# Performance work log

Hardware: AMD Instinct MI355X
Metric: run time of the kernel (lower is better)

Reference implementation:

```python
import jax, jax.numpy as jnp
import numpy as np

# ---- static config (from xib add_argument defaults / chosen production sizes) ----
B, L = 16, 50            # batch, text length
LU, KU, DIM = 60, 100, 60
V, MAXVL = 2000, 10      # vocab size, max vocab word length (J)
MIN_WL, MAX_WL = 4, 10   # min/max extracted word length
NE = MAX_WL - MIN_WL + 1 # number of len_e candidates
INS_DEL_COST = 3.5       # min_ins_del_cost
UNEXTRACTED_PROB = 0.01
CONTEXT_WEIGHT = 0.1     # weight for context (conv) log-probs
NEG = -9999.9


def setup_inputs() -> dict:
    key = jax.random.key(0)
    ks = jax.random.split(key, 8)
    unit_id_seqs = jax.random.randint(ks[0], (B, L), 0, LU)
    lengths = 10 + jax.random.randint(ks[1], (B,), 0, L - 9)  # in [10, L]
    unit_repr = jax.random.normal(ks[2], (KU, DIM), jnp.float32)
    aligner_weight = 0.1 * jax.random.normal(ks[3], (LU, KU), jnp.float32)
    conv_w = jax.random.normal(ks[4], (DIM, DIM, 3), jnp.float32) / np.sqrt(3.0 * DIM)
    conv_b = jnp.zeros((DIM,), jnp.float32)
    vocab_ids = jax.random.randint(ks[5], (V, MAXVL), 0, KU)
    vocab_lengths = MIN_WL + jax.random.randint(ks[6], (V,), 0, MAXVL - MIN_WL + 1)
    return dict(unit_id_seqs=unit_id_seqs, lengths=lengths, unit_repr=unit_repr,
                aligner_weight=aligner_weight, conv_w=conv_w, conv_b=conv_b,
                vocab_ids=vocab_ids, vocab_lengths=vocab_lengths)


def reference(unit_id_seqs, lengths, unit_repr, aligner_weight, conv_w, conv_b,
              vocab_ids, vocab_lengths):
    # ---- G2P layer: embedding-as-matmul + Conv1d over length ----
    ku_char_repr = aligner_weight @ unit_repr                 # (LU, DIM)
    emb = ku_char_repr[unit_id_seqs]                          # (B, L, DIM)
    x = jnp.swapaxes(emb, 1, 2)                               # (B, DIM, L)
    y = jax.lax.conv_general_dilated(x, conv_w, (1,), 'SAME',
                                     dimension_numbers=('NCH', 'OIH', 'NCH'))
    word_repr = jnp.swapaxes(y + conv_b[None, :, None], 1, 2)  # (B, L, DIM)
    char_log_probs = jax.nn.log_softmax(ku_char_repr @ unit_repr.T, axis=-1)  # (LU, KU)
    alignment = jnp.exp(char_log_probs)
    ctx_log_probs = jax.nn.log_softmax(word_repr @ unit_repr.T, axis=-1)      # (B, L, KU)
    # per-position substitution log prob against each known unit
    pos_lp = char_log_probs[unit_id_seqs] + CONTEXT_WEIGHT * ctx_log_probs    # (B, L, KU)
    sub = pos_lp[:, :, vocab_ids]                                             # (B, L, V, J)
    sub = jnp.pad(sub, ((0, 0), (0, MAX_WL), (0, 0), (0, 0)), constant_values=NEG)
    J = MAXVL
    # ---- edit-distance style DP over (span char i, vocab char j), vectorized
    # over (batch, start position, vocab). prev[b,s,j,v] = f[i-1][j].
    j_ar = jnp.arange(J + 1, dtype=sub.dtype)
    prev = jnp.broadcast_to((-INS_DEL_COST * j_ar)[None, None, :, None], (B, L, J + 1, V))
    vl_idx = jnp.broadcast_to(vocab_lengths[None, None, None, :].astype(jnp.int32), (B, L, 1, V))
    lls = []
    for i in range(1, MAX_WL + 1):          # fixed small loop (<=10)
        sub_i = sub[:, i - 1:i - 1 + L]     # (B, L, V, J): char at position s+i-1
        row = [jnp.full((B, L, V), -INS_DEL_COST * i, dtype=sub.dtype)]
        for j in range(1, J + 1):           # fixed small loop (<=10)
            diag = prev[:, :, j - 1, :] + sub_i[:, :, :, j - 1]
            up = prev[:, :, j, :] - INS_DEL_COST
            left = row[j - 1] - INS_DEL_COST
            row.append(jnp.maximum(diag, jnp.maximum(up, left)))
        prev = jnp.stack(row, axis=2)       # (B, L, J+1, V)
        if i >= MIN_WL:                     # matched ll for word length i
            lls.append(jnp.take_along_axis(prev, vl_idx, axis=2)[:, :, 0, :])
    ll = jnp.stack(lls, axis=2)             # (B, L, NE, V) = matches.ll
    # ---- viability mask + unextracted penalty, pick best candidate ----
    starts = jnp.arange(L)
    word_lens = MIN_WL + jnp.arange(NE)
    viable = (starts[None, :, None] + word_lens[None, None, :]) <= lengths[:, None, None]  # (B,L,NE)
    unextracted = (lengths[:, None, None] - word_lens[None, None, :]).astype(ll.dtype)     # (B,1,NE)
    score = (ll + jnp.where(viable, 0.0, NEG)[..., None]
             + (unextracted * np.log(UNEXTRACTED_PROB))[..., None, :, None][:, 0])
    flat = score.reshape(B, L * NE * V)
    best_idx = jnp.argmax(flat, axis=1)
    best_matched_ll = jnp.max(flat, axis=1)
    start = best_idx // (NE * V)
    e_idx = (best_idx // V) % NE
    best_matched_vocab = best_idx % V
    end = start + MIN_WL + e_idx - 1
    return start, end, best_matched_ll, best_matched_vocab, alignment
```

## Files before the change

### kernel.cpp

```cpp
#include <hip/hip_runtime.h>
#include <math.h>
#include <stdint.h>

#define B_ 16
#define L_ 50
#define LU_ 60
#define KU_ 100
#define DIM_ 60
#define V_ 2000
#define MAXVL_ 10
#define MIN_WL_ 4
#define MAX_WL_ 10
#define NE_ 7
#define IDC_ 3.5f
#define LOG_UNEXT_ (-4.6051701859880913680359829093687f)
#define CTXW_ 0.1f
#define NQ_ 13

#define WS_PLP  0
#define WS_BEST_BYTES (80000u * 4u)
#define BEST_STRIDE 8
#define WS_VPACK_BYTES (WS_BEST_BYTES + 1024u)

#define URP_ 61
#define CWP_ 61
#define TSP_ 12

__global__ __launch_bounds__(256) void ctx_kernel(
    const int* __restrict__ uid,
    const float* __restrict__ unit_repr,
    const float* __restrict__ aligner_w,
    const float* __restrict__ conv_w,
    const float* __restrict__ conv_b,
    const int* __restrict__ vocab_ids,
    const int* __restrict__ vocab_lengths,
    float* __restrict__ ws_plp,
    float* __restrict__ out_align,
    unsigned long long* __restrict__ g_best,
    int* __restrict__ vpack)
{
  int blk = blockIdx.x;
  int t = threadIdx.x;

  if (blk == B_ * NQ_) {
    __shared__ unsigned cnt[NE_];
    if (t < NE_) cnt[t] = 0u;
    __syncthreads();
    for (int v = t; v < V_; v += 256)
      atomicAdd(&cnt[vocab_lengths[v] - MIN_WL_], 1u);
    __syncthreads();
    if (t == 0) {
      unsigned s = 0;
      for (int e = 0; e < NE_; ++e) { unsigned c = cnt[e]; cnt[e] = s; s += c; }
    }
    __syncthreads();
    for (int v = t; v < V_; v += 256) {
      int vl = vocab_lengths[v];
      unsigned dst = atomicAdd(&cnt[vl - MIN_WL_], 1u);
      unsigned q0 = 0u, q1 = 0u, q2 = 0u;
#pragma unroll
      for (int j = 0; j < 4; ++j) q0 |= ((unsigned)vocab_ids[v * MAXVL_ + j]) << (j * 8);
#pragma unroll
      for (int j = 0; j < 4; ++j) q1 |= ((unsigned)vocab_ids[v * MAXVL_ + 4 + j]) << (j * 8);
#pragma unroll
      for (int j = 0; j < 2; ++j) q2 |= ((unsigned)vocab_ids[v * MAXVL_ + 8 + j]) << (j * 8);
      int4 w;
      w.x = (int)q0; w.y = (int)q1; w.z = (int)q2;
      w.w = (int)((unsigned)vl | ((unsigned)v << 8));
      ((int4*)vpack)[dst] = w;
    }
    return;
  }

  int b = blk / NQ_, q = blk % NQ_;
  int l0 = 4 * q;
  int npos = (l0 + 4 <= L_) ? 4 : (L_ - l0);
  int alr = (blk < LU_) ? blk : -1;

  __shared__ float s_ur[KU_ * URP_];
  __shared__ float s_cw[3 * DIM_ * CWP_];
  __shared__ float s_aw[7 * KU_];
  __shared__ float s_kx[7 * DIM_];
  __shared__ float swr[4 * DIM_];
  __shared__ float sclp[4 * KU_];
  __shared__ float sctx[4 * KU_];
  __shared__ float salg[KU_];
  __shared__ float sls[9];

  if (blk == 0 && t < B_) g_best[t * BEST_STRIDE] = 0ull;

  const float4* ur4 = (const float4*)unit_repr;
  for (int k = t; k < (KU_ * DIM_) / 4; k += 256) {
    float4 v = ur4[k];
    int i0 = 4 * k;
    s_ur[((i0 + 0) / DIM_) * URP_ + ((i0 + 0) % DIM_)] = v.x;
    s_ur[((i0 + 1) / DIM_) * URP_ + ((i0 + 1) % DIM_)] = v.y;
    s_ur[((i0 + 2) / DIM_) * URP_ + ((i0 + 2) % DIM_)] = v.z;
    s_ur[((i0 + 3) / DIM_) * URP_ + ((i0 + 3) % DIM_)] = v.w;
  }
  const float4* cw4 = (const float4*)conv_w;
  for (int k = t; k < (DIM_ * DIM_ * 3) / 4; k += 256) {
    float4 v = cw4[k];
    int i0 = 4 * k;
    float vv[4] = {v.x, v.y, v.z, v.w};
#pragma unroll
    for (int e = 0; e < 4; ++e) {
      int idx = i0 + e;
      int o = idx / (3 * DIM_), id = idx % (3 * DIM_);
      s_cw[id * CWP_ + o] = vv[e];
    }
  }
  for (int i = t; i < 7 * KU_; i += 256) {
    int m = i / KU_, k = i - m * KU_;
    float w = 0.f;
    if (m < 6) {
      int ld = l0 - 1 + m;
      if (ld >= 0 && ld < L_) {
        int u = uid[b * L_ + ld];
        w = aligner_w[u * KU_ + k];
      }
    } else if (alr >= 0) {
      w = aligner_w[alr * KU_ + k];
    }
    s_aw[i] = w;
  }
  __syncthreads();

  for (int idx = t; idx < 7 * DIM_; idx += 256) {
    int m = idx / DIM_, c = idx - m * DIM_;
    const float4* aw4 = (const float4*)&s_aw[m * KU_];
    float acc = 0.f;
    for (int k4 = 0; k4 < KU_ / 4; ++k4) {
      float4 a = aw4[k4];
      int k = 4 * k4;
      acc += a.x * s_ur[(k + 0) * URP_ + c];
      acc += a.y * s_ur[(k + 1) * URP_ + c];
      acc += a.z * s_ur[(k + 2) * URP_ + c];
      acc += a.w * s_ur[(k + 3) * URP_ + c];
    }
    s_kx[idx] = acc;
  }
  __syncthreads();

  for (int idx = t; idx < 240 + 4 * KU_; idx += 256) {
    if (idx < 240) {
      int p = idx / DIM_, o = idx - p * DIM_;
      const float4* x04 = (const float4*)&s_kx[(p + 0) * DIM_];
      const float4* x14 = (const float4*)&s_kx[(p + 1) * DIM_];
      const float4* x24 = (const float4*)&s_kx[(p + 2) * DIM_];
      float acc = conv_b[o];
      for (int i4 = 0; i4 < DIM_ / 4; ++i4) {
        float4 x0 = x04[i4], x1 = x14[i4], x2 = x24[i4];
        int i = 4 * i4;
        acc += x0.x * s_cw[((i + 0) * 3 + 0) * CWP_ + o];
        acc += x1.x * s_cw[((i + 0) * 3 + 1) * CWP_ + o];
        acc += x2.x * s_cw[((i + 0) * 3 + 2) * CWP_ + o];
        acc += x0.y * s_cw[((i + 1) * 3 + 0) * CWP_ + o];
        acc += x1.y * s_cw[((i + 1) * 3 + 1) * CWP_ + o];
        acc += x2.y * s_cw[((i + 1) * 3 + 2) * CWP_ + o];
        acc += x0.z * s_cw[((i + 2) * 3 + 0) * CWP_ + o];
        acc += x1.z * s_cw[((i + 2) * 3 + 1) * CWP_ + o];
        acc += x2.z * s_cw[((i + 2) * 3 + 2) * CWP_ + o];
        acc += x0.w * s_cw[((i + 3) * 3 + 0) * CWP_ + o];
        acc += x1.w * s_cw[((i + 3) * 3 + 1) * CWP_ + o];
        acc += x2.w * s_cw[((i + 3) * 3 + 2) * CWP_ + o];
      }
      swr[p * DIM_ + o] = acc;
    } else {
      int r = idx - 240;
      int p = r / KU_, j = r - p * KU_;
      const float4* kx4 = (const float4*)&s_kx[(p + 1) * DIM_];
      float acc = 0.f;
      for (int d4 = 0; d4 < DIM_ / 4; ++d4) {
        float4 x = kx4[d4];
        int d = 4 * d4;
        acc += x.x * s_ur[j * URP_ + d + 0];
        acc += x.y * s_ur[j * URP_ + d + 1];
        acc += x.z * s_ur[j * URP_ + d + 2];
        acc += x.w * s_ur[j * URP_ + d + 3];
      }
      sclp[r] = acc;
    }
  }
  __syncthreads();

  for (int idx = t; idx < 4 * KU_ + KU_; idx += 256) {
    if (idx < 4 * KU_) {
      int p = idx / KU_, j = idx - p * KU_;
      const float4* w4 = (const float4*)&swr[p * DIM_];
      float acc = 0.f;
      for (int d4 = 0; d4 < DIM_ / 4; ++d4) {
        float4 x = w4[d4];
        int d = 4 * d4;
        acc += x.x * s_ur[j * URP_ + d + 0];
        acc += x.y * s_ur[j * URP_ + d + 1];
        acc += x.z * s_ur[j * URP_ + d + 2];
        acc += x.w * s_ur[j * URP_ + d + 3];
      }
      sctx[idx] = acc;
    } else {
      int j = idx - 4 * KU_;
      const float4* kx4 = (const float4*)&s_kx[6 * DIM_];
      float acc = 0.f;
      for (int d4 = 0; d4 < DIM_ / 4; ++d4) {
        float4 x = kx4[d4];
        int d = 4 * d4;
        acc += x.x * s_ur[j * URP_ + d + 0];
        acc += x.y * s_ur[j * URP_ + d + 1];
        acc += x.z * s_ur[j * URP_ + d + 2];
        acc += x.w * s_ur[j * URP_ + d + 3];
      }
      salg[j] = acc;
    }
  }
  __syncthreads();

  {
    int g = t >> 5, lane = t & 31;
#pragma unroll
    for (int round = 0; round < 2; ++round) {
      int r = round * 8 + g;
      if (r < 9) {
        const float* arr = (r == 8) ? salg
                          : ((r & 1) ? &sctx[(r >> 1) * KU_] : &sclp[(r >> 1) * KU_]);
        float v1 = arr[lane];
        float v2 = arr[32 + lane];
        float v3 = arr[64 + lane];
        float v4 = (lane < KU_ - 96) ? arr[96 + lane] : -1e30f;
        float mx = fmaxf(fmaxf(v1, v2), fmaxf(v3, v4));
#pragma unroll
        for (int off = 16; off > 0; off >>= 1)
          mx = fmaxf(mx, __shfl_xor(mx, off));
        float s = expf(v1 - mx) + expf(v2 - mx) + expf(v3 - mx) +
                  ((lane < KU_ - 96) ? expf(v4 - mx) : 0.f);
#pragma unroll
        for (int off = 16; off > 0; off >>= 1)
          s += __shfl_xor(s, off);
        if (lane == 0) sls[r] = mx + logf(s);
      }
    }
  }
  __syncthreads();

  for (int idx = t; idx < 4 * KU_; idx += 256) {
    int p = idx / KU_, j = idx - p * KU_;
    if (p < npos) {
      float pos = (sclp[idx] - sls[2 * p]) + CTXW_ * (sctx[idx] - sls[2 * p + 1]);
      ws_plp[(b * L_ + l0 + p) * KU_ + j] = pos;
    }
  }
  if (alr >= 0 && t < KU_)
    out_align[alr * KU_ + t] = expf(salg[t] - sls[8]);
}

__global__ __launch_bounds__(256) void dp_kernel(
    const int* __restrict__ lengths,
    const float* __restrict__ ws_plp,
    const int* __restrict__ vpack,
    unsigned long long* __restrict__ g_best)
{
  int bl = blockIdx.x;
  int b = bl / L_, l = bl % L_;
  int len_b = lengths[b];
  int imax = len_b - l;
  if (imax > MAX_WL_) imax = MAX_WL_;
  if (imax < MIN_WL_) return;

  __shared__ float sT[KU_ * TSP_];
  __shared__ unsigned long long swave[4];
  int t = threadIdx.x;
  {
    int n = imax * KU_;
    for (int idx = t; idx < n; idx += 256) {
      int i = idx / KU_, k = idx - i * KU_;
      sT[k * TSP_ + i] = ws_plp[(bl + i) * KU_ + k];
    }
  }
  __syncthreads();

  int p = blockIdx.y * 256 + t;
  const int4* vp4 = (const int4*)vpack;
  int4 w0 = (2 * p < V_) ? vp4[2 * p] : make_int4(0, 0, 0, 0);
  int4 w1 = (2 * p + 1 < V_) ? vp4[2 * p + 1] : make_int4(0, 0, 0, 0);
  unsigned p0[3] = {(unsigned)w0.x, (unsigned)w0.y, (unsigned)w0.z};
  unsigned p1[3] = {(unsigned)w1.x, (unsigned)w1.y, (unsigned)w1.z};
  int vlen0 = (int)((unsigned)w0.w & 0xFFu);
  int vlen1 = (int)((unsigned)w1.w & 0xFFu);
  int v0 = (int)(((unsigned)w0.w) >> 8);
  int v1 = (int)(((unsigned)w1.w) >> 8);
  int jmax = (vlen0 > vlen1) ? vlen0 : vlen1;

  float A0[MAXVL_ + 1], A1[MAXVL_ + 1];
#pragma unroll
  for (int i = 0; i <= MAXVL_; ++i) {
    A0[i] = -IDC_ * (float)i;
    A1[i] = A0[i];
  }
  unsigned long long bestKey = 0ull;

#pragma unroll
  for (int j = 1; j <= MAXVL_; ++j) {
    if (j <= jmax) {
      int k0 = (int)((p0[(j - 1) >> 2] >> (((j - 1) & 3) * 8)) & 0xFFu);
      int k1 = (int)((p1[(j - 1) >> 2] >> (((j - 1) & 3) * 8)) & 0xFFu);
      const float* c0 = &sT[k0 * TSP_];
      const float* c1 = &sT[k1 * TSP_];
      float4 a0 = *(const float4*)(c0);
      float4 m0 = *(const float4*)(c0 + 4);
      float2 e0 = *(const float2*)(c0 + 8);
      float4 a1 = *(const float4*)(c1);
      float4 m1 = *(const float4*)(c1 + 4);
      float2 e1 = *(const float2*)(c1 + 8);
      float s0[MAXVL_] = {a0.x, a0.y, a0.z, a0.w, m0.x, m0.y, m0.z, m0.w, e0.x, e0.y};
      float s1[MAXVL_] = {a1.x, a1.y, a1.z, a1.w, m1.x, m1.y, m1.z, m1.w, e1.x, e1.y};
      float B0[MAXVL_ + 1], B1[MAXVL_ + 1];
      B0[0] = -IDC_ * (float)j;
      B1[0] = B0[0];
#pragma unroll
      for (int i = 1; i <= MAXVL_; ++i) {
        B0[i] = fmaxf(A0[i - 1] + s0[i - 1], fmaxf(A0[i], B0[i - 1]) - IDC_);
        B1[i] = fmaxf(A1[i - 1] + s1[i - 1], fmaxf(A1[i], B1[i - 1]) - IDC_);
      }
      if (j == vlen0) {
#pragma unroll
        for (int e = 0; e < NE_; ++e) {
          int i = MIN_WL_ + e;
          if (i <= imax) {
            float score = B0[i] + (float)(len_b - i) * LOG_UNEXT_;
            unsigned int idx = (unsigned int)(l * (NE_ * V_) + e * V_ + v0);
            unsigned int u = __float_as_uint(score);
            u = (u & 0x80000000u) ? ~u : (u | 0x80000000u);
            unsigned long long key =
                ((unsigned long long)u << 32) | (unsigned long long)(~idx);
            if (key > bestKey) bestKey = key;
          }
        }
      }
      if (j == vlen1) {
#pragma unroll
        for (int e = 0; e < NE_; ++e) {
          int i = MIN_WL_ + e;
          if (i <= imax) {
            float score = B1[i] + (float)(len_b - i) * LOG_UNEXT_;
            unsigned int idx = (unsigned int)(l * (NE_ * V_) + e * V_ + v1);
            unsigned int u = __float_as_uint(score);
            u = (u & 0x80000000u) ? ~u : (u | 0x80000000u);
            unsigned long long key =
                ((unsigned long long)u << 32) | (unsigned long long)(~idx);
            if (key > bestKey) bestKey = key;
          }
        }
      }
#pragma unroll
      for (int i = 0; i <= MAXVL_; ++i) { A0[i] = B0[i]; A1[i] = B1[i]; }
    }
  }

#pragma unroll
  for (int off = 32; off > 0; off >>= 1) {
    unsigned long long o = __shfl_down(bestKey, off);
    if (o > bestKey) bestKey = o;
  }
  int wid = t >> 6;
  if ((t & 63) == 0) swave[wid] = bestKey;
  __syncthreads();
  if (t == 0) {
    unsigned long long k0 = swave[0];
    for (int w = 1; w < 4; ++w)
      if (swave[w] > k0) k0 = swave[w];
    atomicMax(g_best + (size_t)b * BEST_STRIDE, k0);
  }
}

__global__ void decode_kernel(const unsigned long long* __restrict__ g_best,
                              float* __restrict__ out)
{
  int t = threadIdx.x;
  if (t < B_) {
    unsigned long long key = g_best[t * BEST_STRIDE];
    unsigned int u = (unsigned int)(key >> 32);
    unsigned int idx = ~((unsigned int)(key & 0xFFFFFFFFull));
    unsigned int bits = (u & 0x80000000u) ? (u & 0x7FFFFFFFu) : ~u;
    float val = __uint_as_float(bits);
    int start = (int)(idx / (NE_ * V_));
    int rem = (int)(idx % (NE_ * V_));
    int e = rem / V_;
    int vv = rem % V_;
    out[t] = (float)start;
    out[B_ + t] = (float)(start + MIN_WL_ + e - 1);
    out[2 * B_ + t] = val;
    out[3 * B_ + t] = (float)vv;
  }
}

extern "C" void kernel_launch(void* const* d_in, const int* in_sizes, int n_in,
                              void* d_out, int out_size, void* d_ws, size_t ws_size,
                              hipStream_t stream)
{
  const int* uid            = (const int*)d_in[0];
  const int* lengths        = (const int*)d_in[1];
  const float* unit_repr    = (const float*)d_in[2];
  const float* aligner_w    = (const float*)d_in[3];
  const float* conv_w       = (const float*)d_in[4];
  const float* conv_b       = (const float*)d_in[5];
  const int* vocab_ids      = (const int*)d_in[6];
  const int* vocab_lengths  = (const int*)d_in[7];
  float* out = (float*)d_out;
  float* ws_f = (float*)d_ws;
  unsigned long long* g_best =
      (unsigned long long*)((char*)d_ws + WS_BEST_BYTES);
  int* vpack = (int*)((char*)d_ws + WS_VPACK_BYTES);

  ctx_kernel<<<B_ * NQ_ + 1, 256, 0, stream>>>(uid, unit_repr, aligner_w,
                                               conv_w, conv_b, vocab_ids,
                                               vocab_lengths, ws_f + WS_PLP,
                                               out + 4 * B_, g_best, vpack);
  dim3 g3(B_ * L_, 4);
  dp_kernel<<<g3, 256, 0, stream>>>(lengths, ws_f + WS_PLP, vpack, g_best);
  decode_kernel<<<1, 64, 0, stream>>>(g_best, out);
}
```

Baseline: 102.3 us.

## Halve DP grid with two vocab passes per block and transpose unit_repr in LDS

The DP kernel grid drops from 4 to 2 blocks per (batch, start), and each thread runs two passes over vocab pairs. This spreads the per-block cost of staging the score table into shared memory over twice as many vocab words. The ctx kernel also keeps a transposed copy of unit_repr in shared memory so the embedding matmul can use float4 loads on both operands. The costs are fewer blocks available for parallelism and more shared memory in the ctx kernel.

```diff
diff --git a/kernel.cpp b/kernel.cpp
--- a/kernel.cpp
+++ b/kernel.cpp
@@ -78,6 +78,7 @@
   int alr = (blk < LU_) ? blk : -1;
 
   __shared__ float s_ur[KU_ * URP_];
+  __shared__ float s_urT[DIM_ * KU_];
   __shared__ float s_cw[3 * DIM_ * CWP_];
   __shared__ float s_aw[7 * KU_];
   __shared__ float s_kx[7 * DIM_];
@@ -93,10 +94,14 @@
   for (int k = t; k < (KU_ * DIM_) / 4; k += 256) {
     float4 v = ur4[k];
     int i0 = 4 * k;
-    s_ur[((i0 + 0) / DIM_) * URP_ + ((i0 + 0) % DIM_)] = v.x;
-    s_ur[((i0 + 1) / DIM_) * URP_ + ((i0 + 1) % DIM_)] = v.y;
-    s_ur[((i0 + 2) / DIM_) * URP_ + ((i0 + 2) % DIM_)] = v.z;
-    s_ur[((i0 + 3) / DIM_) * URP_ + ((i0 + 3) % DIM_)] = v.w;
+    float vv[4] = {v.x, v.y, v.z, v.w};
+#pragma unroll
+    for (int e = 0; e < 4; ++e) {
+      int idx = i0 + e;
+      int kr = idx / DIM_, c = idx % DIM_;
+      s_ur[kr * URP_ + c] = vv[e];
+      s_urT[c * KU_ + kr] = vv[e];
+    }
   }
   const float4* cw4 = (const float4*)conv_w;
   for (int k = t; k < (DIM_ * DIM_ * 3) / 4; k += 256) {
@@ -129,14 +134,11 @@
   for (int idx = t; idx < 7 * DIM_; idx += 256) {
     int m = idx / DIM_, c = idx - m * DIM_;
     const float4* aw4 = (const float4*)&s_aw[m * KU_];
+    const float4* ut4 = (const float4*)&s_urT[c * KU_];
     float acc = 0.f;
     for (int k4 = 0; k4 < KU_ / 4; ++k4) {
-      float4 a = aw4[k4];
-      int k = 4 * k4;
-      acc += a.x * s_ur[(k + 0) * URP_ + c];
-      acc += a.y * s_ur[(k + 1) * URP_ + c];
-      acc += a.z * s_ur[(k + 2) * URP_ + c];
-      acc += a.w * s_ur[(k + 3) * URP_ + c];
+      float4 a = aw4[k4], u = ut4[k4];
+      acc += a.x * u.x + a.y * u.y + a.z * u.z + a.w * u.w;
     }
     s_kx[idx] = acc;
   }
@@ -278,81 +280,84 @@
   }
   __syncthreads();
 
-  int p = blockIdx.y * 256 + t;
   const int4* vp4 = (const int4*)vpack;
-  int4 w0 = (2 * p < V_) ? vp4[2 * p] : make_int4(0, 0, 0, 0);
-  int4 w1 = (2 * p + 1 < V_) ? vp4[2 * p + 1] : make_int4(0, 0, 0, 0);
-  unsigned p0[3] = {(unsigned)w0.x, (unsigned)w0.y, (unsigned)w0.z};
-  unsigned p1[3] = {(unsigned)w1.x, (unsigned)w1.y, (unsigned)w1.z};
-  int vlen0 = (int)((unsigned)w0.w & 0xFFu);
-  int vlen1 = (int)((unsigned)w1.w & 0xFFu);
-  int v0 = (int)(((unsigned)w0.w) >> 8);
-  int v1 = (int)(((unsigned)w1.w) >> 8);
-  int jmax = (vlen0 > vlen1) ? vlen0 : vlen1;
-
-  float A0[MAXVL_ + 1], A1[MAXVL_ + 1];
-#pragma unroll
-  for (int i = 0; i <= MAXVL_; ++i) {
-    A0[i] = -IDC_ * (float)i;
-    A1[i] = A0[i];
-  }
   unsigned long long bestKey = 0ull;
 
-#pragma unroll
-  for (int j = 1; j <= MAXVL_; ++j) {
-    if (j <= jmax) {
-      int k0 = (int)((p0[(j - 1) >> 2] >> (((j - 1) & 3) * 8)) & 0xFFu);
-      int k1 = (int)((p1[(j - 1) >> 2] >> (((j - 1) & 3) * 8)) & 0xFFu);
-      const float* c0 = &sT[k0 * TSP_];
-      const float* c1 = &sT[k1 * TSP_];
-      float4 a0 = *(const float4*)(c0);
-      float4 m0 = *(const float4*)(c0 + 4);
-      float2 e0 = *(const float2*)(c0 + 8);
-      float4 a1 = *(const float4*)(c1);
-      float4 m1 = *(const float4*)(c1 + 4);
-      float2 e1 = *(const float2*)(c1 + 8);
-      float s0[MAXVL_] = {a0.x, a0.y, a0.z, a0.w, m0.x, m0.y, m0.z, m0.w, e0.x, e0.y};
-      float s1[MAXVL_] = {a1.x, a1.y, a1.z, a1.w, m1.x, m1.y, m1.z, m1.w, e1.x, e1.y};
-      float B0[MAXVL_ + 1], B1[MAXVL_ + 1];
-      B0[0] = -IDC_ * (float)j;
-      B1[0] = B0[0];
-#pragma unroll
-      for (int i = 1; i <= MAXVL_; ++i) {
-        B0[i] = fmaxf(A0[i - 1] + s0[i - 1], fmaxf(A0[i], B0[i - 1]) - IDC_);
-        B1[i] = fmaxf(A1[i - 1] + s1[i - 1], fmaxf(A1[i], B1[i - 1]) - IDC_);
-      }
-      if (j == vlen0) {
-#pragma unroll
-        for (int e = 0; e < NE_; ++e) {
-          int i = MIN_WL_ + e;
-          if (i <= imax) {
-            float score = B0[i] + (float)(len_b - i) * LOG_UNEXT_;
-            unsigned int idx = (unsigned int)(l * (NE_ * V_) + e * V_ + v0);
-            unsigned int u = __float_as_uint(score);
-            u = (u & 0x80000000u) ? ~u : (u | 0x80000000u);
-            unsigned long long key =
-                ((unsigned long long)u << 32) | (unsigned long long)(~idx);
-            if (key > bestKey) bestKey = key;
+  for (int pass = 0; pass < 2; ++pass) {
+    int e0 = blockIdx.y * 1024 + pass * 512 + 2 * t;
+    int4 w0 = (e0 < V_) ? vp4[e0] : make_int4(0, 0, 0, 0);
+    int4 w1 = (e0 + 1 < V_) ? vp4[e0 + 1] : make_int4(0, 0, 0, 0);
+    unsigned p0[3] = {(unsigned)w0.x, (unsigned)w0.y, (unsigned)w0.z};
+    unsigned p1[3] = {(unsigned)w1.x, (unsigned)w1.y, (unsigned)w1.z};
+    int vlen0 = (int)((unsigned)w0.w & 0xFFu);
+    int vlen1 = (int)((unsigned)w1.w & 0xFFu);
+    int v0 = (int)(((unsigned)w0.w) >> 8);
+    int v1 = (int)(((unsigned)w1.w) >> 8);
+    int jmax = (vlen0 > vlen1) ? vlen0 : vlen1;
+
+    float A0[MAXVL_ + 1], A1[MAXVL_ + 1];
+#pragma unroll
+    for (int i = 0; i <= MAXVL_; ++i) {
+      A0[i] = -IDC_ * (float)i;
+      A1[i] = A0[i];
+    }
+
+#pragma unroll
+    for (int j = 1; j <= MAXVL_; ++j) {
+      if (j <= jmax) {
+        int k0 = (int)((p0[(j - 1) >> 2] >> (((j - 1) & 3) * 8)) & 0xFFu);
+        int k1 = (int)((p1[(j - 1) >> 2] >> (((j - 1) & 3) * 8)) & 0xFFu);
+        const float* c0 = &sT[k0 * TSP_];
+        const float* c1 = &sT[k1 * TSP_];
+        float4 a0 = *(const float4*)(c0);
+        float4 m0 = *(const float4*)(c0 + 4);
+        float2 e0v = *(const float2*)(c0 + 8);
+        float4 a1 = *(const float4*)(c1);
+        float4 m1 = *(const float4*)(c1 + 4);
+        float2 e1v = *(const float2*)(c1 + 8);
+        float s0[MAXVL_] = {a0.x, a0.y, a0.z, a0.w, m0.x, m0.y, m0.z, m0.w, e0v.x, e0v.y};
+        float s1[MAXVL_] = {a1.x, a1.y, a1.z, a1.w, m1.x, m1.y, m1.z, m1.w, e1v.x, e1v.y};
+        float B0[MAXVL_ + 1], B1[MAXVL_ + 1];
+        B0[0] = -IDC_ * (float)j;
+        B1[0] = B0[0];
+#pragma unroll
+        for (int i = 1; i <= MAXVL_; ++i) {
+          B0[i] = fmaxf(A0[i - 1] + s0[i - 1], fmaxf(A0[i], B0[i - 1]) - IDC_);
+          B1[i] = fmaxf(A1[i - 1] + s1[i - 1], fmaxf(A1[i], B1[i - 1]) - IDC_);
+        }
+        if (j == vlen0) {
+#pragma unroll
+          for (int e = 0; e < NE_; ++e) {
+            int i = MIN_WL_ + e;
+            if (i <= imax) {
+              float score = B0[i] + (float)(len_b - i) * LOG_UNEXT_;
+              unsigned int idx = (unsigned int)(l * (NE_ * V_) + e * V_ + v0);
+              unsigned int u = __float_as_uint(score);
+              u = (u & 0x80000000u) ? ~u : (u | 0x80000000u);
+              unsigned long long key =
+                  ((unsigned long long)u << 32) | (unsigned long long)(~idx);
+              if (key > bestKey) bestKey = key;
+            }
           }
         }
-      }
-      if (j == vlen1) {
-#pragma unroll
-        for (int e = 0; e < NE_; ++e) {
-          int i = MIN_WL_ + e;
-          if (i <= imax) {
-            float score = B1[i] + (float)(len_b - i) * LOG_UNEXT_;
-            unsigned int idx = (unsigned int)(l * (NE_ * V_) + e * V_ + v1);
-            unsigned int u = __float_as_uint(score);
-            u = (u & 0x80000000u) ? ~u : (u | 0x80000000u);
-            unsigned long long key =
-                ((unsigned long long)u << 32) | (unsigned long long)(~idx);
-            if (key > bestKey) bestKey = key;
+        if (j == vlen1) {
+#pragma unroll
+          for (int e = 0; e < NE_; ++e) {
+            int i = MIN_WL_ + e;
+            if (i <= imax) {
+              float score = B1[i] + (float)(len_b - i) * LOG_UNEXT_;
+              unsigned int idx = (unsigned int)(l * (NE_ * V_) + e * V_ + v1);
+              unsigned int u = __float_as_uint(score);
+              u = (u & 0x80000000u) ? ~u : (u | 0x80000000u);
+              unsigned long long key =
+                  ((unsigned long long)u << 32) | (unsigned long long)(~idx);
+              if (key > bestKey) bestKey = key;
+            }
           }
         }
-      }
-#pragma unroll
-      for (int i = 0; i <= MAXVL_; ++i) { A0[i] = B0[i]; A1[i] = B1[i]; }
+#pragma unroll
+        for (int i = 0; i <= MAXVL_; ++i) { A0[i] = B0[i]; A1[i] = B1[i]; }
+      }
     }
   }
 
@@ -415,7 +420,7 @@
                                                conv_w, conv_b, vocab_ids,
                                                vocab_lengths, ws_f + WS_PLP,
                                                out + 4 * B_, g_best, vpack);
-  dim3 g3(B_ * L_, 4);
+  dim3 g3(B_ * L_, 2);
   dp_kernel<<<g3, 256, 0, stream>>>(lengths, ws_f + WS_PLP, vpack, g_best);
   decode_kernel<<<1, 64, 0, stream>>>(g_best, out);
 }
```

Measured after the change: 103.2 us, median of 2. Within noise of the previous version (+0.8%).
